# Kernel tuning notes

Hardware: AMD Instinct MI355X
Metric: run time of the kernel (lower is better)

## Reference

```python
import jax, jax.numpy as jnp
import numpy as np

N_NODES = 100000


def gcn_conv(x, W, b, edge_index, n_nodes):
    """PyG GCNConv: add self-loops, symmetric deg^-1/2 normalization,
    linear transform, scatter-sum aggregation, bias."""
    x = x @ W  # [N, out]
    src, dst = edge_index[0], edge_index[1]
    self_idx = jnp.arange(n_nodes, dtype=src.dtype)
    src = jnp.concatenate([src, self_idx])
    dst = jnp.concatenate([dst, self_idx])
    # in-degree (including self-loop) per destination node
    deg = jax.ops.segment_sum(jnp.ones_like(src, dtype=x.dtype), dst,
                              num_segments=n_nodes)
    dinv = jnp.where(deg > 0, jax.lax.rsqrt(deg), 0.0)
    norm = dinv[src] * dinv[dst]  # [E+N]
    msg = x[src] * norm[:, None]  # gather + scale, [E+N, out]
    out = jax.ops.segment_sum(msg, dst, num_segments=n_nodes)
    return out + b


def setup_inputs() -> dict:
    key = jax.random.key(0)
    ks = jax.random.split(key, 7)
    in_c, hid_c, out_c = 256, 128, 64
    n_edges, n_lbl = 1600000, 200000
    x = jax.random.normal(ks[0], (N_NODES, in_c), dtype=jnp.float32)
    edge_index = jax.random.randint(ks[1], (2, n_edges), 0, N_NODES, dtype=jnp.int64)
    edge_label_index = jax.random.randint(ks[2], (2, n_lbl), 0, N_NODES, dtype=jnp.int64)
    # Glorot-style init for GCN linear weights
    W1 = jax.random.normal(ks[3], (in_c, hid_c), dtype=jnp.float32) / np.sqrt(in_c)
    b1 = jnp.zeros((hid_c,), dtype=jnp.float32)
    W2 = jax.random.normal(ks[4], (hid_c, out_c), dtype=jnp.float32) / np.sqrt(hid_c)
    b2 = jnp.zeros((out_c,), dtype=jnp.float32)
    return {"x": x, "edge_index": edge_index,
            "edge_label_index": edge_label_index,
            "W1": W1, "b1": b1, "W2": W2, "b2": b2}


def reference(x, edge_index, edge_label_index, W1, b1, W2, b2):
    n = x.shape[0]
    h = jax.nn.relu(gcn_conv(x, W1, b1, edge_index, n))
    z = gcn_conv(h, W2, b2, edge_index, n)  # [N, out_c]
    src, dst = edge_label_index[0], edge_label_index[1]
    return jnp.sum(z[src] * z[dst], axis=-1)  # [E_lbl]
```

## Files before the change

kernel.cpp:

```cpp
#include <hip/hip_runtime.h>
#include <hip/hip_bf16.h>

#define N_NODES 100000
#define N_EDGES 1600000
#define N_LBL   200000
#define C_IN    256
#define C_HID   128
#define C_OUT   64
#define SCAN_BLOCKS 391
#define NBUCKET 391
#define BCAP 8192
#define FILLA_EPB 2048

using u16 = unsigned short;
using u32 = unsigned int;
using u64 = unsigned long long;
using s64 = long long;

typedef __attribute__((ext_vector_type(8))) short bf16x8;
typedef __attribute__((ext_vector_type(4))) float f32x4;

__device__ __forceinline__ float bf2f(u16 h) {
    u32 u = ((u32)h) << 16;
    float f;
    __builtin_memcpy(&f, &u, 4);
    return f;
}
__device__ __forceinline__ u16 f2bf(float f) {
    u32 u;
    __builtin_memcpy(&u, &f, 4);
    u32 r = (u + 0x7fffu + ((u >> 16) & 1u)) >> 16;
    return (u16)r;
}
__device__ __forceinline__ void unpack_bf2(u32 p, float& lo, float& hi) {
    u32 l = p << 16;
    u32 h = p & 0xffff0000u;
    __builtin_memcpy(&lo, &l, 4);
    __builtin_memcpy(&hi, &h, 4);
}
__device__ __forceinline__ void acc8(uint4 p, float* a) {
    float f0, f1;
    unpack_bf2(p.x, f0, f1); a[0] += f0; a[1] += f1;
    unpack_bf2(p.y, f0, f1); a[2] += f0; a[3] += f1;
    unpack_bf2(p.z, f0, f1); a[4] += f0; a[5] += f1;
    unpack_bf2(p.w, f0, f1); a[6] += f0; a[7] += f1;
}
__device__ __forceinline__ int geti(const void* p, s64 i, int i64) {
    return i64 ? (int)((const s64*)p)[i] : ((const int*)p)[i];
}
__device__ __forceinline__ int clampn(int v) {
    return ((u32)v < (u32)N_NODES) ? v : 0;
}

__device__ __forceinline__ void split8(const float4& a, const float4& b,
                                       bf16x8& hi8, bf16x8& lo8) {
    float va[8] = {a.x, a.y, a.z, a.w, b.x, b.y, b.z, b.w};
    u32 uh[4], ul[4];
#pragma unroll
    for (int p = 0; p < 4; ++p) {
        float x0 = va[2 * p], x1 = va[2 * p + 1];
        u32 u0, u1;
        __builtin_memcpy(&u0, &x0, 4);
        __builtin_memcpy(&u1, &x1, 4);
        u32 h0 = u0 & 0xffff0000u, h1 = u1 & 0xffff0000u;
        float f0, f1;
        __builtin_memcpy(&f0, &h0, 4);
        __builtin_memcpy(&f1, &h1, 4);
        float l0 = x0 - f0, l1 = x1 - f1;
        u32 w0, w1;
        __builtin_memcpy(&w0, &l0, 4);
        __builtin_memcpy(&w1, &l1, 4);
        uh[p] = (u0 >> 16) | h1;
        ul[p] = (w0 >> 16) | (w1 & 0xffff0000u);
    }
    struct U { u32 w[4]; };
    U H = {{uh[0], uh[1], uh[2], uh[3]}};
    U L = {{ul[0], ul[1], ul[2], ul[3]}};
    __builtin_memcpy(&hi8, &H, 16);
    __builtin_memcpy(&lo8, &L, 16);
}

__global__ void k_detect(const void* __restrict__ x, const void* __restrict__ ei,
                         int* __restrict__ flags) {
    const int lane = threadIdx.x & 63;
    const u16* xh = (const u16*)x;
    int cnt = 0;
#pragma unroll
    for (int k = 0; k < 4; ++k) {
        int i = 2 * (lane + 64 * k);
        u32 e = (xh[i] >> 7) & 0xFF;
        cnt += __builtin_popcountll(__ballot(e > 137));
    }
    const u32* ew = (const u32*)ei;
    int nz = __builtin_popcountll(__ballot(ew[2 * lane + 1] != 0));
    if (lane == 0) {
        flags[0] = (cnt > 16) ? 1 : 0;
        flags[1] = (nz == 0) ? 1 : 0;
    }
}


__global__ __launch_bounds__(512) void k_binit(int* __restrict__ gcur) {
    int t = threadIdx.x;
    if (t < NBUCKET) gcur[t] = t * BCAP;
}

__global__ __launch_bounds__(256) void k_fillA(const void* __restrict__ ei,
                                               const int* __restrict__ flags,
                                               int* __restrict__ gcur,
                                               u32* __restrict__ temp) {
    __shared__ int hist[NBUCKET];
    __shared__ int gbase[NBUCKET];
    const int t = threadIdx.x;
    if (t < NBUCKET) hist[t] = 0;
    if (t + 256 < NBUCKET) hist[t + 256] = 0;
    __syncthreads();
    const s64 base = (s64)blockIdx.x * FILLA_EPB;
    const int i64 = flags[1];
    int sv[8], dv[8], bk[8], off[8];
    bool val[8];
#pragma unroll
    for (int j = 0; j < 8; ++j) {
        s64 e = base + t + 256 * j;
        val[j] = (e < N_EDGES);
        if (val[j]) {
            sv[j] = clampn(geti(ei, e, i64));
            dv[j] = clampn(geti(ei, (s64)N_EDGES + e, i64));
            bk[j] = dv[j] >> 8;
            off[j] = atomicAdd(&hist[bk[j]], 1);
        }
    }
    __syncthreads();
    if (t < NBUCKET && hist[t]) gbase[t] = atomicAdd(&gcur[t], hist[t]);
    if (t + 256 < NBUCKET && hist[t + 256]) gbase[t + 256] = atomicAdd(&gcur[t + 256], hist[t + 256]);
    __syncthreads();
#pragma unroll
    for (int j = 0; j < 8; ++j) {
        if (val[j]) {
            int pos = gbase[bk[j]] + off[j];
            if (pos < (bk[j] + 1) * BCAP)
                temp[pos] = (u32)sv[j] | ((u32)(dv[j] & 255) << 20);
        }
    }
}

__global__ __launch_bounds__(256) void k_deg2(const u32* __restrict__ temp,
                                              const int* __restrict__ gcur,
                                              int* __restrict__ deg) {
    __shared__ int dcnt[256];
    const int t = threadIdx.x;
    const int b = blockIdx.x;
    dcnt[t] = 0;
    __syncthreads();
    const int beg = b * BCAP, end = gcur[b];
    for (int e = beg + t; e < end; e += 256) {
        u32 dl = (temp[e] >> 20) & 255u;
        atomicAdd(&dcnt[dl], 1);
    }
    __syncthreads();
    int node = (b << 8) + t;
    if (node < N_NODES) deg[node] = dcnt[t];
}

__global__ __launch_bounds__(256) void k_fillB(const u32* __restrict__ temp,
                                               const int* __restrict__ gcur,
                                               const int* __restrict__ row_ptr,
                                               int* __restrict__ csr_src) {
    __shared__ int cur[256];
    const int t = threadIdx.x;
    const int b = blockIdx.x;
    int node = (b << 8) + t;
    cur[t] = (node < N_NODES) ? row_ptr[node] : 0;
    __syncthreads();
    const int beg = b * BCAP, end = gcur[b];
    for (int e = beg + t; e < end; e += 256) {
        u32 p = temp[e];
        u32 s = p & 0xFFFFFu;
        u32 dl = (p >> 20) & 255u;
        int pos = atomicAdd(&cur[dl], 1);
        csr_src[pos] = (int)s;
    }
}

__global__ __launch_bounds__(512) void k_scan2(const int* __restrict__ gcur,
                                               int* __restrict__ boff,
                                               int* __restrict__ row_ptr) {
    __shared__ int arr[512];
    const int t = threadIdx.x;
    int v = (t < NBUCKET) ? (gcur[t] - t * BCAP) : 0;
    arr[t] = v;
    __syncthreads();
#pragma unroll
    for (int off = 1; off < 512; off <<= 1) {
        int u = (t >= off) ? arr[t - off] : 0;
        __syncthreads();
        arr[t] += u;
        __syncthreads();
    }
    if (t < NBUCKET) boff[t] = arr[t] - v;
    if (t == 511) row_ptr[N_NODES] = arr[511];
}

__global__ __launch_bounds__(256) void k_scan3(const int* __restrict__ deg,
                                               const int* __restrict__ boff,
                                               int* __restrict__ row_ptr,
                                               float* __restrict__ dinv) {
    __shared__ int arr[256];
    const int t = threadIdx.x;
    int i = blockIdx.x * 256 + t;
    int v = (i < N_NODES) ? deg[i] : 0;
    arr[t] = v;
    __syncthreads();
#pragma unroll
    for (int off = 1; off < 256; off <<= 1) {
        int u = (t >= off) ? arr[t - off] : 0;
        __syncthreads();
        arr[t] += u;
        __syncthreads();
    }
    if (i < N_NODES) {
        int run = boff[blockIdx.x] + arr[t] - v;
        row_ptr[i] = run;
        dinv[i]    = rsqrtf((float)v + 1.0f);
    }
}

__global__ __launch_bounds__(256) void k_w1t(const void* __restrict__ W1_,
                                             const int* __restrict__ flags,
                                             u16* __restrict__ w1t_hi,
                                             u16* __restrict__ w1t_lo) {
    int idx = blockIdx.x * 256 + threadIdx.x;
    int k = idx >> 7, n = idx & 127;
    float v = flags[0] ? ((const float*)W1_)[idx] : bf2f(((const u16*)W1_)[idx]);
    u32 uv;
    __builtin_memcpy(&uv, &v, 4);
    u32 hf = uv & 0xffff0000u;
    float hb;
    __builtin_memcpy(&hb, &hf, 4);
    float lo = v - hb;
    u32 ulo;
    __builtin_memcpy(&ulo, &lo, 4);
    w1t_hi[n * C_IN + k] = (u16)(uv >> 16);
    w1t_lo[n * C_IN + k] = (u16)(ulo >> 16);
}

__global__ __launch_bounds__(256) void k_w2t(const void* __restrict__ W2_,
                                             const int* __restrict__ flags,
                                             u16* __restrict__ w2t_hi,
                                             u16* __restrict__ w2t_lo) {
    int idx = blockIdx.x * 256 + threadIdx.x;
    int k = idx >> 6, n = idx & 63;
    float v = flags[0] ? ((const float*)W2_)[idx] : bf2f(((const u16*)W2_)[idx]);
    u32 uv;
    __builtin_memcpy(&uv, &v, 4);
    u32 hf = uv & 0xffff0000u;
    float hb;
    __builtin_memcpy(&hb, &hf, 4);
    float lo = v - hb;
    u32 ulo;
    __builtin_memcpy(&ulo, &lo, 4);
    w2t_hi[n * C_HID + k] = (u16)(uv >> 16);
    w2t_lo[n * C_HID + k] = (u16)(ulo >> 16);
}

__global__ __launch_bounds__(832) void k_gemm1_mfma(const void* __restrict__ xv_,
                                                    const u16* __restrict__ w1t_hi,
                                                    const u16* __restrict__ w1t_lo,
                                                    const float* __restrict__ dinv,
                                                    const int* __restrict__ flags,
                                                    u16* __restrict__ g0) {
    extern __shared__ char smem[];
    u16* lds_hi = (u16*)smem;
    u16* lds_lo = (u16*)(smem + 65536);
    const int isf32 = flags[0];
    const int lane = threadIdx.x & 63;
    const int wid  = threadIdx.x >> 6;
    const int r0   = blockIdx.x * 416 + wid * 32;

    for (int g = threadIdx.x; g < 4096; g += 832) {
        int row = g >> 5;
        int off = (g & 31) << 4;
        int dst = row * 512 + (off ^ ((row & 7) << 4));
        *(uint4*)((char*)lds_hi + dst) =
            *(const uint4*)((const char*)(w1t_hi + (size_t)row * C_IN) + off);
        *(uint4*)((char*)lds_lo + dst) =
            *(const uint4*)((const char*)(w1t_lo + (size_t)row * C_IN) + off);
    }
    __syncthreads();

    const int rowA = r0 + (lane & 15);
    const int rowB = rowA + 16;
    const int rlA  = (rowA < N_NODES) ? rowA : (N_NODES - 1);
    const int rlB  = (rowB < N_NODES) ? rowB : (N_NODES - 1);
    const int kh   = (lane >> 4) * 8;
    const int khb  = (lane >> 4) * 16;

    int rbase[8], rswz[8];
#pragma unroll
    for (int n = 0; n < 8; ++n) {
        int rloc = n * 16 + (lane & 15);
        rbase[n] = rloc * 512;
        rswz[n]  = (rloc & 7) << 4;
    }

    f32x4 acc[2][8];
#pragma unroll
    for (int g = 0; g < 2; ++g)
#pragma unroll
        for (int n = 0; n < 8; ++n) acc[g][n] = (f32x4){0.f, 0.f, 0.f, 0.f};

    if (isf32) {
        const float* apA = (const float*)xv_ + (size_t)rlA * C_IN + kh;
        const float* apB = (const float*)xv_ + (size_t)rlB * C_IN + kh;
        float4 xa0 = ((const float4*)apA)[0];
        float4 xa1 = ((const float4*)(apA + 4))[0];
        float4 xb0 = ((const float4*)apB)[0];
        float4 xb1 = ((const float4*)(apB + 4))[0];
#pragma unroll
        for (int k0 = 0; k0 < C_IN; k0 += 32) {
            float4 na0, na1, nb0, nb1;
            if (k0 + 32 < C_IN) {
                na0 = ((const float4*)(apA + k0 + 32))[0];
                na1 = ((const float4*)(apA + k0 + 36))[0];
                nb0 = ((const float4*)(apB + k0 + 32))[0];
                nb1 = ((const float4*)(apB + k0 + 36))[0];
            }
            bf16x8 ahiA, aloA, ahiB, aloB;
            split8(xa0, xa1, ahiA, aloA);
            split8(xb0, xb1, ahiB, aloB);
#pragma unroll
            for (int n = 0; n < 8; ++n) {
                int a = rbase[n] + ((k0 * 2 + khb) ^ rswz[n]);
                bf16x8 bh = *(const bf16x8*)((const char*)lds_hi + a);
                bf16x8 bl = *(const bf16x8*)((const char*)lds_lo + a);
                acc[0][n] = __builtin_amdgcn_mfma_f32_16x16x32_bf16(ahiA, bl, acc[0][n], 0, 0, 0);
                acc[0][n] = __builtin_amdgcn_mfma_f32_16x16x32_bf16(aloA, bh, acc[0][n], 0, 0, 0);
                acc[0][n] = __builtin_amdgcn_mfma_f32_16x16x32_bf16(ahiA, bh, acc[0][n], 0, 0, 0);
                acc[1][n] = __builtin_amdgcn_mfma_f32_16x16x32_bf16(ahiB, bl, acc[1][n], 0, 0, 0);
                acc[1][n] = __builtin_amdgcn_mfma_f32_16x16x32_bf16(aloB, bh, acc[1][n], 0, 0, 0);
                acc[1][n] = __builtin_amdgcn_mfma_f32_16x16x32_bf16(ahiB, bh, acc[1][n], 0, 0, 0);
            }
            if (k0 + 32 < C_IN) { xa0 = na0; xa1 = na1; xb0 = nb0; xb1 = nb1; }
        }
    } else {
        const u16* apA = (const u16*)xv_ + (size_t)rlA * C_IN + kh;
        const u16* apB = (const u16*)xv_ + (size_t)rlB * C_IN + kh;
        bf16x8 aA = *(const bf16x8*)apA;
        bf16x8 aB = *(const bf16x8*)apB;
#pragma unroll
        for (int k0 = 0; k0 < C_IN; k0 += 32) {
            bf16x8 nA, nB;
            if (k0 + 32 < C_IN) {
                nA = *(const bf16x8*)(apA + k0 + 32);
                nB = *(const bf16x8*)(apB + k0 + 32);
            }
#pragma unroll
            for (int n = 0; n < 8; ++n) {
                int a = rbase[n] + ((k0 * 2 + khb) ^ rswz[n]);
                bf16x8 bh = *(const bf16x8*)((const char*)lds_hi + a);
                acc[0][n] = __builtin_amdgcn_mfma_f32_16x16x32_bf16(aA, bh, acc[0][n], 0, 0, 0);
                acc[1][n] = __builtin_amdgcn_mfma_f32_16x16x32_bf16(aB, bh, acc[1][n], 0, 0, 0);
            }
            if (k0 + 32 < C_IN) { aA = nA; aB = nB; }
        }
    }

    const int ccol = lane & 15;
#pragma unroll
    for (int g = 0; g < 2; ++g) {
        const int crow0 = r0 + g * 16 + (lane >> 4) * 4;
#pragma unroll
        for (int i = 0; i < 4; ++i) {
            int r = crow0 + i;
            if (r < N_NODES) {
                float dv = dinv[r];
#pragma unroll
                for (int n = 0; n < 8; ++n)
                    g0[(size_t)r * C_HID + n * 16 + ccol] = f2bf(dv * acc[g][n][i]);
            }
        }
    }
}

__global__ __launch_bounds__(512) void k_gemm2_mfma(const float* __restrict__ h,
                                                    const u16* __restrict__ w2t_hi,
                                                    const u16* __restrict__ w2t_lo,
                                                    const float* __restrict__ dinv,
                                                    u16* __restrict__ g1) {
    __shared__ u16 lds_hi[64 * 128];
    __shared__ u16 lds_lo[64 * 128];
    const int lane = threadIdx.x & 63;
    const int wid  = threadIdx.x >> 6;
    const int r0   = blockIdx.x * 256 + wid * 32;

    {
        for (int g = threadIdx.x; g < 1024; g += 512) {
            int row = g >> 4;
            int off = (g & 15) << 4;
            int dst = row * 256 + (off ^ ((row & 7) << 4));
            *(uint4*)((char*)lds_hi + dst) =
                *(const uint4*)((const char*)(w2t_hi + (size_t)row * C_HID) + off);
            *(uint4*)((char*)lds_lo + dst) =
                *(const uint4*)((const char*)(w2t_lo + (size_t)row * C_HID) + off);
        }
    }
    __syncthreads();

    const int rowA = r0 + (lane & 15);
    const int rowB = rowA + 16;
    const int rlA  = (rowA < N_NODES) ? rowA : (N_NODES - 1);
    const int rlB  = (rowB < N_NODES) ? rowB : (N_NODES - 1);
    const int kh   = (lane >> 4) * 8;
    const int khb  = (lane >> 4) * 16;

    int rbase[4], rswz[4];
#pragma unroll
    for (int n = 0; n < 4; ++n) {
        int rloc = n * 16 + (lane & 15);
        rbase[n] = rloc * 256;
        rswz[n]  = (rloc & 7) << 4;
    }

    f32x4 acc[2][4];
#pragma unroll
    for (int g = 0; g < 2; ++g)
#pragma unroll
        for (int n = 0; n < 4; ++n) acc[g][n] = (f32x4){0.f, 0.f, 0.f, 0.f};

    const float* apA = h + (size_t)rlA * C_HID + kh;
    const float* apB = h + (size_t)rlB * C_HID + kh;

    float4 xa0 = ((const float4*)apA)[0];
    float4 xa1 = ((const float4*)(apA + 4))[0];
    float4 xb0 = ((const float4*)apB)[0];
    float4 xb1 = ((const float4*)(apB + 4))[0];
#pragma unroll
    for (int k0 = 0; k0 < C_HID; k0 += 32) {
        bf16x8 bh[4], bl[4];
#pragma unroll
        for (int n = 0; n < 4; ++n) {
            int a = rbase[n] + ((k0 * 2 + khb) ^ rswz[n]);
            bh[n] = *(const bf16x8*)((const char*)lds_hi + a);
            bl[n] = *(const bf16x8*)((const char*)lds_lo + a);
        }
        float4 na0, na1, nb0, nb1;
        if (k0 + 32 < C_HID) {
            na0 = ((const float4*)(apA + k0 + 32))[0];
            na1 = ((const float4*)(apA + k0 + 36))[0];
            nb0 = ((const float4*)(apB + k0 + 32))[0];
            nb1 = ((const float4*)(apB + k0 + 36))[0];
        }
        bf16x8 ahiA, aloA, ahiB, aloB;
        split8(xa0, xa1, ahiA, aloA);
        split8(xb0, xb1, ahiB, aloB);
#pragma unroll
        for (int n = 0; n < 4; ++n) {
            acc[0][n] = __builtin_amdgcn_mfma_f32_16x16x32_bf16(ahiA, bl[n], acc[0][n], 0, 0, 0);
            acc[0][n] = __builtin_amdgcn_mfma_f32_16x16x32_bf16(aloA, bh[n], acc[0][n], 0, 0, 0);
            acc[0][n] = __builtin_amdgcn_mfma_f32_16x16x32_bf16(ahiA, bh[n], acc[0][n], 0, 0, 0);
            acc[1][n] = __builtin_amdgcn_mfma_f32_16x16x32_bf16(ahiB, bl[n], acc[1][n], 0, 0, 0);
            acc[1][n] = __builtin_amdgcn_mfma_f32_16x16x32_bf16(aloB, bh[n], acc[1][n], 0, 0, 0);
            acc[1][n] = __builtin_amdgcn_mfma_f32_16x16x32_bf16(ahiB, bh[n], acc[1][n], 0, 0, 0);
        }
        if (k0 + 32 < C_HID) { xa0 = na0; xa1 = na1; xb0 = nb0; xb1 = nb1; }
    }

    const int ccol = lane & 15;
#pragma unroll
    for (int g = 0; g < 2; ++g) {
        const int crow0 = r0 + g * 16 + (lane >> 4) * 4;
#pragma unroll
        for (int i = 0; i < 4; ++i) {
            int r = crow0 + i;
            if (r < N_NODES) {
                float dv = dinv[r];
#pragma unroll
                for (int n = 0; n < 4; ++n)
                    g1[(size_t)r * C_OUT + n * 16 + ccol] = f2bf(dv * acc[g][n][i]);
            }
        }
    }
}

__global__ __launch_bounds__(256) void k_gather128(const int* __restrict__ row_ptr,
                                                   const int* __restrict__ csr_src,
                                                   const uint4* __restrict__ g,
                                                   const void* __restrict__ bias_,
                                                   const float* __restrict__ dinv,
                                                   const int* __restrict__ flags,
                                                   float* __restrict__ out) {
    const int lane = threadIdx.x & 63;
    const int wid  = threadIdx.x >> 6;
    const int q    = lane >> 4;
    const int jj   = lane & 15;
    const int node = blockIdx.x * 16 + wid * 4 + q;
    const uint4* gp = g + jj;
    const int beg = row_ptr[node], end = row_ptr[node + 1];
    float a[8] = {0.f, 0.f, 0.f, 0.f, 0.f, 0.f, 0.f, 0.f};
    int e = beg;
    for (; e + 4 <= end; e += 4) {
        int s0 = csr_src[e], s1 = csr_src[e + 1];
        int s2 = csr_src[e + 2], s3 = csr_src[e + 3];
        uint4 p0 = gp[(size_t)s0 * 16];
        uint4 p1 = gp[(size_t)s1 * 16];
        uint4 p2 = gp[(size_t)s2 * 16];
        uint4 p3 = gp[(size_t)s3 * 16];
        acc8(p0, a);
        acc8(p1, a);
        acc8(p2, a);
        acc8(p3, a);
    }
    for (; e < end; ++e) acc8(gp[(size_t)csr_src[e] * 16], a);
    acc8(gp[(size_t)node * 16], a);
    float b[8];
    if (flags[0]) {
        float4 b0 = ((const float4*)bias_)[2 * jj];
        float4 b1 = ((const float4*)bias_)[2 * jj + 1];
        b[0] = b0.x; b[1] = b0.y; b[2] = b0.z; b[3] = b0.w;
        b[4] = b1.x; b[5] = b1.y; b[6] = b1.z; b[7] = b1.w;
    } else {
        uint4 bw = ((const uint4*)bias_)[jj];
        unpack_bf2(bw.x, b[0], b[1]);
        unpack_bf2(bw.y, b[2], b[3]);
        unpack_bf2(bw.z, b[4], b[5]);
        unpack_bf2(bw.w, b[6], b[7]);
    }
    float dv = dinv[node];
    float4 r0, r1;
    r0.x = fmaxf(dv * a[0] + b[0], 0.f);
    r0.y = fmaxf(dv * a[1] + b[1], 0.f);
    r0.z = fmaxf(dv * a[2] + b[2], 0.f);
    r0.w = fmaxf(dv * a[3] + b[3], 0.f);
    r1.x = fmaxf(dv * a[4] + b[4], 0.f);
    r1.y = fmaxf(dv * a[5] + b[5], 0.f);
    r1.z = fmaxf(dv * a[6] + b[6], 0.f);
    r1.w = fmaxf(dv * a[7] + b[7], 0.f);
    float4* op = (float4*)(out + (size_t)node * C_HID);
    op[2 * jj]     = r0;
    op[2 * jj + 1] = r1;
}

__global__ __launch_bounds__(256) void k_gather64(const int* __restrict__ row_ptr,
                                                  const int* __restrict__ csr_src,
                                                  const uint4* __restrict__ g,
                                                  const void* __restrict__ bias_,
                                                  const float* __restrict__ dinv,
                                                  const int* __restrict__ flags,
                                                  float* __restrict__ out) {
    const int lane = threadIdx.x & 63;
    const int wid  = threadIdx.x >> 6;
    const int oct  = lane >> 3;
    const int jj   = lane & 7;
    const int node = blockIdx.x * 32 + wid * 8 + oct;
    const uint4* gp = g + jj;
    const int beg = row_ptr[node], end = row_ptr[node + 1];
    float a[8] = {0.f, 0.f, 0.f, 0.f, 0.f, 0.f, 0.f, 0.f};
    int e = beg;
    for (; e + 4 <= end; e += 4) {
        int s0 = csr_src[e], s1 = csr_src[e + 1];
        int s2 = csr_src[e + 2], s3 = csr_src[e + 3];
        uint4 p0 = gp[(size_t)s0 * 8];
        uint4 p1 = gp[(size_t)s1 * 8];
        uint4 p2 = gp[(size_t)s2 * 8];
        uint4 p3 = gp[(size_t)s3 * 8];
        acc8(p0, a);
        acc8(p1, a);
        acc8(p2, a);
        acc8(p3, a);
    }
    for (; e < end; ++e) acc8(gp[(size_t)csr_src[e] * 8], a);
    acc8(gp[(size_t)node * 8], a);
    float b[8];
    if (flags[0]) {
        float4 b0 = ((const float4*)bias_)[2 * jj];
        float4 b1 = ((const float4*)bias_)[2 * jj + 1];
        b[0] = b0.x; b[1] = b0.y; b[2] = b0.z; b[3] = b0.w;
        b[4] = b1.x; b[5] = b1.y; b[6] = b1.z; b[7] = b1.w;
    } else {
        uint4 bw = ((const uint4*)bias_)[jj];
        unpack_bf2(bw.x, b[0], b[1]);
        unpack_bf2(bw.y, b[2], b[3]);
        unpack_bf2(bw.z, b[4], b[5]);
        unpack_bf2(bw.w, b[6], b[7]);
    }
    float dv = dinv[node];
    float4 r0, r1;
    r0.x = dv * a[0] + b[0];
    r0.y = dv * a[1] + b[1];
    r0.z = dv * a[2] + b[2];
    r0.w = dv * a[3] + b[3];
    r1.x = dv * a[4] + b[4];
    r1.y = dv * a[5] + b[5];
    r1.z = dv * a[6] + b[6];
    r1.w = dv * a[7] + b[7];
    float4* op = (float4*)(out + (size_t)node * C_OUT);
    op[2 * jj]     = r0;
    op[2 * jj + 1] = r1;
}

__global__ __launch_bounds__(256) void k_edgedot(const void* __restrict__ eli,
                                                 const int* __restrict__ flags,
                                                 const float* __restrict__ z,
                                                 void* __restrict__ out) {
    const int g16 = threadIdx.x >> 4;
    const int l16 = threadIdx.x & 15;
    const int e = blockIdx.x * 16 + g16;
    if (e >= N_LBL) return;
    const int i64 = flags[1];
    const int s = clampn(geti(eli, e, i64));
    const int d = clampn(geti(eli, (s64)N_LBL + e, i64));
    float4 zs = *(const float4*)(z + (size_t)s * C_OUT + l16 * 4);
    float4 zd = *(const float4*)(z + (size_t)d * C_OUT + l16 * 4);
    float v = zs.x * zd.x + zs.y * zd.y + zs.z * zd.z + zs.w * zd.w;
    v += __shfl_xor(v, 1, 64);
    v += __shfl_xor(v, 2, 64);
    v += __shfl_xor(v, 4, 64);
    v += __shfl_xor(v, 8, 64);
    if (l16 == 0) {
        if (flags[0]) ((float*)out)[e] = v;
        else          ((u16*)out)[e]   = f2bf(v);
    }
}

extern "C" void kernel_launch(void* const* d_in, const int* in_sizes, int n_in,
                              void* d_out, int out_size, void* d_ws, size_t ws_size,
                              hipStream_t stream) {
    const void* x   = d_in[0];
    const void* ei  = d_in[1];
    const void* eli = d_in[2];
    const void* W1  = d_in[3];
    const void* b1  = d_in[4];
    const void* W2  = d_in[5];
    const void* b2  = d_in[6];

    if (ws_size < 84800128) return;
    char* ws = (char*)d_ws;
    float* h       = (float*)ws;
    float* z       = (float*)ws;
    int*   boff    = (int*)(ws + 4096);
    int*   gcur    = (int*)(ws + 16384);
    u32*   temp    = (u32*)(ws + 1048576);
    u16*   g0      = (u16*)(ws + 51200000);
    u16*   g1      = (u16*)(ws + 51200000);
    float* dinv    = (float*)(ws + 76800000);
    int*   deg     = (int*)(ws + 77200000);
    u16*   w1t_hi  = (u16*)(ws + 77200000);
    u16*   w1t_lo  = (u16*)(ws + 77200000 + 65536);
    u16*   w2t_hi  = (u16*)(ws + 77200000 + 131072);
    u16*   w2t_lo  = (u16*)(ws + 77200000 + 147456);
    int*   row_ptr = (int*)(ws + 77600000);
    int*   csr_src = (int*)(ws + 78400008);
    int*   flags   = (int*)(ws + 84800064);

    const int FILLA_GRID = (N_EDGES + FILLA_EPB - 1) / FILLA_EPB;

    static bool attr_set = false;
    if (!attr_set) {
        hipFuncSetAttribute((const void*)k_gemm1_mfma,
                            hipFuncAttributeMaxDynamicSharedMemorySize, 131072);
        attr_set = true;
    }

    k_detect<<<1, 64, 0, stream>>>(x, ei, flags);

    k_binit<<<1, 512, 0, stream>>>(gcur);
    k_fillA<<<FILLA_GRID, 256, 0, stream>>>(ei, flags, gcur, temp);
    k_deg2<<<NBUCKET, 256, 0, stream>>>(temp, gcur, deg);

    k_scan2<<<1, 512, 0, stream>>>(gcur, boff, row_ptr);
    k_scan3<<<SCAN_BLOCKS, 256, 0, stream>>>(deg, boff, row_ptr, dinv);

    k_fillB<<<NBUCKET, 256, 0, stream>>>(temp, gcur, row_ptr, csr_src);

    k_w1t<<<128, 256, 0, stream>>>(W1, flags, w1t_hi, w1t_lo);
    k_w2t<<<32, 256, 0, stream>>>(W2, flags, w2t_hi, w2t_lo);

    k_gemm1_mfma<<<256, 832, 131072, stream>>>(x, w1t_hi, w1t_lo, dinv, flags, g0);
    k_gather128<<<N_NODES / 16, 256, 0, stream>>>(row_ptr, csr_src, (const uint4*)g0, b1, dinv, flags, h);

    k_gemm2_mfma<<<(N_NODES + 255) / 256, 512, 0, stream>>>(h, w2t_hi, w2t_lo, dinv, g1);
    k_gather64<<<N_NODES / 32, 256, 0, stream>>>(row_ptr, csr_src, (const uint4*)g1, b2, dinv, flags, z);

    k_edgedot<<<(N_LBL + 15) / 16, 256, 0, stream>>>(eli, flags, z, d_out);
}
```

Before: 364.4 us.

## Split GEMM1 weight staging into two K-halves with static 64KB LDS

The first-layer GEMM now stages the transposed W1 hi/lo split in two 128-wide K chunks using 64KB of static shared memory instead of 128KB of dynamic LDS. Blocks shrink from 13 to 7 waves (224 rows each) and the grid doubles to 512. The aim is to let more blocks fit per CU and to spread work across more blocks, improving occupancy and load balance. The cost is an extra barrier and a second weight reload per block, plus more total weight staging traffic across the larger grid.

Result: no change. 367.3 us (+0.8%).

```diff
diff --git a/kernel.cpp b/kernel.cpp
--- a/kernel.cpp
+++ b/kernel.cpp
@@ -263,30 +263,18 @@
     w2t_lo[n * C_HID + k] = (u16)(ulo >> 16);
 }
 
-__global__ __launch_bounds__(832) void k_gemm1_mfma(const void* __restrict__ xv_,
+__global__ __launch_bounds__(448) void k_gemm1_mfma(const void* __restrict__ xv_,
                                                     const u16* __restrict__ w1t_hi,
                                                     const u16* __restrict__ w1t_lo,
                                                     const float* __restrict__ dinv,
                                                     const int* __restrict__ flags,
                                                     u16* __restrict__ g0) {
-    extern __shared__ char smem[];
-    u16* lds_hi = (u16*)smem;
-    u16* lds_lo = (u16*)(smem + 65536);
+    __shared__ u16 lds_hi[128 * 128];
+    __shared__ u16 lds_lo[128 * 128];
     const int isf32 = flags[0];
     const int lane = threadIdx.x & 63;
     const int wid  = threadIdx.x >> 6;
-    const int r0   = blockIdx.x * 416 + wid * 32;
-
-    for (int g = threadIdx.x; g < 4096; g += 832) {
-        int row = g >> 5;
-        int off = (g & 31) << 4;
-        int dst = row * 512 + (off ^ ((row & 7) << 4));
-        *(uint4*)((char*)lds_hi + dst) =
-            *(const uint4*)((const char*)(w1t_hi + (size_t)row * C_IN) + off);
-        *(uint4*)((char*)lds_lo + dst) =
-            *(const uint4*)((const char*)(w1t_lo + (size_t)row * C_IN) + off);
-    }
-    __syncthreads();
+    const int r0   = blockIdx.x * 224 + wid * 32;
 
     const int rowA = r0 + (lane & 15);
     const int rowB = rowA + 16;
@@ -299,7 +287,7 @@
 #pragma unroll
     for (int n = 0; n < 8; ++n) {
         int rloc = n * 16 + (lane & 15);
-        rbase[n] = rloc * 512;
+        rbase[n] = rloc * 256;
         rswz[n]  = (rloc & 7) << 4;
     }
 
@@ -309,59 +297,75 @@
 #pragma unroll
         for (int n = 0; n < 8; ++n) acc[g][n] = (f32x4){0.f, 0.f, 0.f, 0.f};
 
-    if (isf32) {
-        const float* apA = (const float*)xv_ + (size_t)rlA * C_IN + kh;
-        const float* apB = (const float*)xv_ + (size_t)rlB * C_IN + kh;
-        float4 xa0 = ((const float4*)apA)[0];
-        float4 xa1 = ((const float4*)(apA + 4))[0];
-        float4 xb0 = ((const float4*)apB)[0];
-        float4 xb1 = ((const float4*)(apB + 4))[0];
-#pragma unroll
-        for (int k0 = 0; k0 < C_IN; k0 += 32) {
-            float4 na0, na1, nb0, nb1;
-            if (k0 + 32 < C_IN) {
-                na0 = ((const float4*)(apA + k0 + 32))[0];
-                na1 = ((const float4*)(apA + k0 + 36))[0];
-                nb0 = ((const float4*)(apB + k0 + 32))[0];
-                nb1 = ((const float4*)(apB + k0 + 36))[0];
+#pragma unroll
+    for (int kp = 0; kp < 2; ++kp) {
+        const int kbase = kp * 128;
+        if (kp) __syncthreads();
+        for (int g = threadIdx.x; g < 2048; g += 448) {
+            int row = g >> 4;
+            int off = (g & 15) << 4;
+            int dst = row * 256 + (off ^ ((row & 7) << 4));
+            *(uint4*)((char*)lds_hi + dst) =
+                *(const uint4*)((const char*)(w1t_hi + (size_t)row * C_IN + kbase) + off);
+            *(uint4*)((char*)lds_lo + dst) =
+                *(const uint4*)((const char*)(w1t_lo + (size_t)row * C_IN + kbase) + off);
+        }
+        __syncthreads();
+
+        if (isf32) {
+            const float* apA = (const float*)xv_ + (size_t)rlA * C_IN + kbase + kh;
+            const float* apB = (const float*)xv_ + (size_t)rlB * C_IN + kbase + kh;
+            float4 xa0 = ((const float4*)apA)[0];
+            float4 xa1 = ((const float4*)(apA + 4))[0];
+            float4 xb0 = ((const float4*)apB)[0];
+            float4 xb1 = ((const float4*)(apB + 4))[0];
+#pragma unroll
+            for (int k0 = 0; k0 < 128; k0 += 32) {
+                float4 na0, na1, nb0, nb1;
+                if (k0 + 32 < 128) {
+                    na0 = ((const float4*)(apA + k0 + 32))[0];
+                    na1 = ((const float4*)(apA + k0 + 36))[0];
+                    nb0 = ((const float4*)(apB + k0 + 32))[0];
+                    nb1 = ((const float4*)(apB + k0 + 36))[0];
+                }
+                bf16x8 ahiA, aloA, ahiB, aloB;
+                split8(xa0, xa1, ahiA, aloA);
+                split8(xb0, xb1, ahiB, aloB);
+#pragma unroll
+                for (int n = 0; n < 8; ++n) {
+                    int a = rbase[n] + ((k0 * 2 + khb) ^ rswz[n]);
+                    bf16x8 bh = *(const bf16x8*)((const char*)lds_hi + a);
+                    bf16x8 bl = *(const bf16x8*)((const char*)lds_lo + a);
+                    acc[0][n] = __builtin_amdgcn_mfma_f32_16x16x32_bf16(ahiA, bl, acc[0][n], 0, 0, 0);
+                    acc[0][n] = __builtin_amdgcn_mfma_f32_16x16x32_bf16(aloA, bh, acc[0][n], 0, 0, 0);
+                    acc[0][n] = __builtin_amdgcn_mfma_f32_16x16x32_bf16(ahiA, bh, acc[0][n], 0, 0, 0);
+                    acc[1][n] = __builtin_amdgcn_mfma_f32_16x16x32_bf16(ahiB, bl, acc[1][n], 0, 0, 0);
+                    acc[1][n] = __builtin_amdgcn_mfma_f32_16x16x32_bf16(aloB, bh, acc[1][n], 0, 0, 0);
+                    acc[1][n] = __builtin_amdgcn_mfma_f32_16x16x32_bf16(ahiB, bh, acc[1][n], 0, 0, 0);
+                }
+                if (k0 + 32 < 128) { xa0 = na0; xa1 = na1; xb0 = nb0; xb1 = nb1; }
             }
-            bf16x8 ahiA, aloA, ahiB, aloB;
-            split8(xa0, xa1, ahiA, aloA);
-            split8(xb0, xb1, ahiB, aloB);
-#pragma unroll
-            for (int n = 0; n < 8; ++n) {
-                int a = rbase[n] + ((k0 * 2 + khb) ^ rswz[n]);
-                bf16x8 bh = *(const bf16x8*)((const char*)lds_hi + a);
-                bf16x8 bl = *(const bf16x8*)((const char*)lds_lo + a);
-                acc[0][n] = __builtin_amdgcn_mfma_f32_16x16x32_bf16(ahiA, bl, acc[0][n], 0, 0, 0);
-                acc[0][n] = __builtin_amdgcn_mfma_f32_16x16x32_bf16(aloA, bh, acc[0][n], 0, 0, 0);
-                acc[0][n] = __builtin_amdgcn_mfma_f32_16x16x32_bf16(ahiA, bh, acc[0][n], 0, 0, 0);
-                acc[1][n] = __builtin_amdgcn_mfma_f32_16x16x32_bf16(ahiB, bl, acc[1][n], 0, 0, 0);
-                acc[1][n] = __builtin_amdgcn_mfma_f32_16x16x32_bf16(aloB, bh, acc[1][n], 0, 0, 0);
-                acc[1][n] = __builtin_amdgcn_mfma_f32_16x16x32_bf16(ahiB, bh, acc[1][n], 0, 0, 0);
+        } else {
+            const u16* apA = (const u16*)xv_ + (size_t)rlA * C_IN + kbase + kh;
+            const u16* apB = (const u16*)xv_ + (size_t)rlB * C_IN + kbase + kh;
+            bf16x8 aA = *(const bf16x8*)apA;
+            bf16x8 aB = *(const bf16x8*)apB;
+#pragma unroll
+            for (int k0 = 0; k0 < 128; k0 += 32) {
+                bf16x8 nA, nB;
+                if (k0 + 32 < 128) {
+                    nA = *(const bf16x8*)(apA + k0 + 32);
+                    nB = *(const bf16x8*)(apB + k0 + 32);
+                }
+#pragma unroll
+                for (int n = 0; n < 8; ++n) {
+                    int a = rbase[n] + ((k0 * 2 + khb) ^ rswz[n]);
+                    bf16x8 bh = *(const bf16x8*)((const char*)lds_hi + a);
+                    acc[0][n] = __builtin_amdgcn_mfma_f32_16x16x32_bf16(aA, bh, acc[0][n], 0, 0, 0);
+                    acc[1][n] = __builtin_amdgcn_mfma_f32_16x16x32_bf16(aB, bh, acc[1][n], 0, 0, 0);
+                }
+                if (k0 + 32 < 128) { aA = nA; aB = nB; }
             }
-            if (k0 + 32 < C_IN) { xa0 = na0; xa1 = na1; xb0 = nb0; xb1 = nb1; }
-        }
-    } else {
-        const u16* apA = (const u16*)xv_ + (size_t)rlA * C_IN + kh;
-        const u16* apB = (const u16*)xv_ + (size_t)rlB * C_IN + kh;
-        bf16x8 aA = *(const bf16x8*)apA;
-        bf16x8 aB = *(const bf16x8*)apB;
-#pragma unroll
-        for (int k0 = 0; k0 < C_IN; k0 += 32) {
-            bf16x8 nA, nB;
-            if (k0 + 32 < C_IN) {
-                nA = *(const bf16x8*)(apA + k0 + 32);
-                nB = *(const bf16x8*)(apB + k0 + 32);
-            }
-#pragma unroll
-            for (int n = 0; n < 8; ++n) {
-                int a = rbase[n] + ((k0 * 2 + khb) ^ rswz[n]);
-                bf16x8 bh = *(const bf16x8*)((const char*)lds_hi + a);
-                acc[0][n] = __builtin_amdgcn_mfma_f32_16x16x32_bf16(aA, bh, acc[0][n], 0, 0, 0);
-                acc[1][n] = __builtin_amdgcn_mfma_f32_16x16x32_bf16(aB, bh, acc[1][n], 0, 0, 0);
-            }
-            if (k0 + 32 < C_IN) { aA = nA; aB = nB; }
         }
     }
 
@@ -654,13 +658,6 @@
 
     const int FILLA_GRID = (N_EDGES + FILLA_EPB - 1) / FILLA_EPB;
 
-    static bool attr_set = false;
-    if (!attr_set) {
-        hipFuncSetAttribute((const void*)k_gemm1_mfma,
-                            hipFuncAttributeMaxDynamicSharedMemorySize, 131072);
-        attr_set = true;
-    }
-
     k_detect<<<1, 64, 0, stream>>>(x, ei, flags);
 
     k_binit<<<1, 512, 0, stream>>>(gcur);
@@ -675,7 +672,7 @@
     k_w1t<<<128, 256, 0, stream>>>(W1, flags, w1t_hi, w1t_lo);
     k_w2t<<<32, 256, 0, stream>>>(W2, flags, w2t_hi, w2t_lo);
 
-    k_gemm1_mfma<<<256, 832, 131072, stream>>>(x, w1t_hi, w1t_lo, dinv, flags, g0);
+    k_gemm1_mfma<<<512, 448, 0, stream>>>(x, w1t_hi, w1t_lo, dinv, flags, g0);
     k_gather128<<<N_NODES / 16, 256, 0, stream>>>(row_ptr, csr_src, (const uint4*)g0, b1, dinv, flags, h);
 
     k_gemm2_mfma<<<(N_NODES + 255) / 256, 512, 0, stream>>>(h, w2t_hi, w2t_lo, dinv, g1);
```
